# Kernel optimization log

Measured on AMD Instinct MI355X. Metric: run time of the kernel, lower is better.

Reference implementation:

```python
import jax, jax.numpy as jnp
import numpy as np

BIAS = (1, 1)


def setup_inputs() -> dict:
    key = jax.random.key(0)
    k1, k2 = jax.random.split(key)
    B, N = 32, 1024
    c = jax.random.normal(k1, (B, 2 * N), dtype=jnp.float32)
    y = jax.random.randint(k2, (B, N), 0, 2, dtype=jnp.int32)
    return {"c": c, "y": y}


def reference(c, y):
    # split_tensor: even columns -> c1 (scores c_{2r}), odd columns -> s1 (thresholds s_{2r+1})
    c1 = c[:, ::2]   # [B, N]
    s1 = c[:, 1::2]  # [B, N]
    yf = y.astype(jnp.float32)
    y_bar = 1.0 - yf

    y_norm = jnp.sum(yf, axis=1) ** BIAS[0]
    y_bar_norm = jnp.sum(y_bar, axis=1) ** BIAS[1]
    denom = 2.0 * y_norm * y_bar_norm + y_norm * y_norm + y_bar_norm * y_bar_norm

    # pairwise_sub_exp(a, b, x) = sum_{k,l} a_k b_l exp(x_l - x_k)
    #                           = (sum_k a_k e^{-x_k}) * (sum_l b_l e^{x_l})  -- fused, no [B,N,N] materialization
    y_exp_neg_c1 = jnp.sum(yf * jnp.exp(-c1), axis=1)      # sum_k y_k e^{-c1_k}
    ybar_exp_c1 = jnp.sum(y_bar * jnp.exp(c1), axis=1)     # sum_l ybar_l e^{c1_l}
    ybar_exp_neg_s1 = jnp.sum(y_bar * jnp.exp(-s1), axis=1)
    y_exp_s1 = jnp.sum(yf * jnp.exp(s1), axis=1)

    p1 = y_exp_neg_c1 * ybar_exp_c1        # pairwise_sub_exp(y, y_bar, c1)
    p2 = ybar_exp_neg_s1 * y_exp_s1        # pairwise_sub_exp(y_bar, y, s1)
    # valueThreshod_sub_exp(a, x, s) = sum_{r,t} a_r a_t exp(s_t - x_r)
    v1 = y_exp_neg_c1 * y_exp_s1           # valueThreshod_sub_exp(y, c1, s1)
    v2 = ybar_exp_neg_s1 * ybar_exp_c1     # valueThreshod_sub_exp(y_bar, s1, c1)

    return jnp.mean((p1 + p2 + v1 + v2) / denom)
```

## Files before the change

kernel.cpp:

```cpp
#include <hip/hip_runtime.h>

#define NCOLS 1024
#define NROWS 32

__global__ __launch_bounds__(1024) void bpmll_fused_kernel(
    const float* __restrict__ c, const int* __restrict__ y,
    float* __restrict__ out) {
    const int tid = threadIdx.x;
    const int wave = tid >> 6;
    const int lane = tid & 63;
    __shared__ float rowv[NROWS];

    #pragma unroll
    for (int rr = 0; rr < 2; ++rr) {
        const int row = wave * 2 + rr;
        const float4* __restrict__ crow4 =
            reinterpret_cast<const float4*>(c + (size_t)row * 2 * NCOLS);
        const int2* __restrict__ yrow2 =
            reinterpret_cast<const int2*>(y + (size_t)row * NCOLS);

        float sy = 0.f, sA = 0.f, sB = 0.f, sC = 0.f, sD = 0.f;
        #pragma unroll
        for (int k = 0; k < 8; ++k) {
            const int idx = k * 64 + lane;
            const float4 F = crow4[idx];
            const int2  Y = yrow2[idx];
            {
                const bool yy = (Y.x != 0);
                const float e1 = __expf(yy ? -F.x : F.x);
                const float e2 = __expf(yy ?  F.y : -F.y);
                sy += yy ? 1.f : 0.f;
                sA += yy ? e1 : 0.f;
                sD += yy ? e2 : 0.f;
                sC += yy ? 0.f : e1;
                sB += yy ? 0.f : e2;
            }
            {
                const bool yy = (Y.y != 0);
                const float e1 = __expf(yy ? -F.z : F.z);
                const float e2 = __expf(yy ?  F.w : -F.w);
                sy += yy ? 1.f : 0.f;
                sA += yy ? e1 : 0.f;
                sD += yy ? e2 : 0.f;
                sC += yy ? 0.f : e1;
                sB += yy ? 0.f : e2;
            }
        }
        #pragma unroll
        for (int off = 32; off > 0; off >>= 1) {
            sy += __shfl_xor(sy, off);
            sA += __shfl_xor(sA, off);
            sB += __shfl_xor(sB, off);
            sC += __shfl_xor(sC, off);
            sD += __shfl_xor(sD, off);
        }
        if (lane == 0) {
            const float yn  = sy;
            const float ybn = (float)NCOLS - sy;
            const float denom = 2.f * yn * ybn + yn * yn + ybn * ybn;
            rowv[row] = (sA + sB) * (sC + sD) / denom;
        }
    }
    __syncthreads();
    if (tid < 64) {
        float v = (lane < NROWS) ? rowv[lane] : 0.f;
        #pragma unroll
        for (int off = 32; off > 0; off >>= 1) v += __shfl_xor(v, off);
        if (lane == 0) out[0] = v * (1.f / NROWS);
    }
}

extern "C" void kernel_launch(void* const* d_in, const int* in_sizes, int n_in,
                              void* d_out, int out_size, void* d_ws, size_t ws_size,
                              hipStream_t stream) {
    const float* c = (const float*)d_in[0];
    const int*   y = (const int*)d_in[1];
    float* out = (float*)d_out;
    (void)d_ws; (void)ws_size;
    bpmll_fused_kernel<<<1, 1024, 0, stream>>>(c, y, out);
}
```

Baseline: 11.60 us.

## Spread rows across 32 blocks with cooperative grid sync for final mean

Replaces the single 1024-thread block with 32 blocks of 256 threads, one per row, so the loads and exponentials run across many compute units instead of one. Per-row partial sums are reduced through shared memory and written to workspace, then a cooperative grid sync lets block 0 compute the mean. This adds the overhead of a cooperative launch and a grid-wide barrier, which can be costly next to such a small amount of work.

```diff
diff --git a/kernel.cpp b/kernel.cpp
--- a/kernel.cpp
+++ b/kernel.cpp
@@ -1,72 +1,85 @@
 #include <hip/hip_runtime.h>
+#include <hip/hip_cooperative_groups.h>
+
+namespace cg = cooperative_groups;
 
 #define NCOLS 1024
 #define NROWS 32
 
-__global__ __launch_bounds__(1024) void bpmll_fused_kernel(
+__global__ __launch_bounds__(256) void bpmll_coop_kernel(
     const float* __restrict__ c, const int* __restrict__ y,
-    float* __restrict__ out) {
+    float* __restrict__ ws, float* __restrict__ out) {
+    const int row = blockIdx.x;
     const int tid = threadIdx.x;
     const int wave = tid >> 6;
     const int lane = tid & 63;
-    __shared__ float rowv[NROWS];
 
+    const float4* __restrict__ crow4 =
+        reinterpret_cast<const float4*>(c + (size_t)row * 2 * NCOLS);
+    const int2* __restrict__ yrow2 =
+        reinterpret_cast<const int2*>(y + (size_t)row * NCOLS);
+
+    float sy = 0.f, sA = 0.f, sB = 0.f, sC = 0.f, sD = 0.f;
     #pragma unroll
-    for (int rr = 0; rr < 2; ++rr) {
-        const int row = wave * 2 + rr;
-        const float4* __restrict__ crow4 =
-            reinterpret_cast<const float4*>(c + (size_t)row * 2 * NCOLS);
-        const int2* __restrict__ yrow2 =
-            reinterpret_cast<const int2*>(y + (size_t)row * NCOLS);
-
-        float sy = 0.f, sA = 0.f, sB = 0.f, sC = 0.f, sD = 0.f;
-        #pragma unroll
-        for (int k = 0; k < 8; ++k) {
-            const int idx = k * 64 + lane;
-            const float4 F = crow4[idx];
-            const int2  Y = yrow2[idx];
-            {
-                const bool yy = (Y.x != 0);
-                const float e1 = __expf(yy ? -F.x : F.x);
-                const float e2 = __expf(yy ?  F.y : -F.y);
-                sy += yy ? 1.f : 0.f;
-                sA += yy ? e1 : 0.f;
-                sD += yy ? e2 : 0.f;
-                sC += yy ? 0.f : e1;
-                sB += yy ? 0.f : e2;
-            }
-            {
-                const bool yy = (Y.y != 0);
-                const float e1 = __expf(yy ? -F.z : F.z);
-                const float e2 = __expf(yy ?  F.w : -F.w);
-                sy += yy ? 1.f : 0.f;
-                sA += yy ? e1 : 0.f;
-                sD += yy ? e2 : 0.f;
-                sC += yy ? 0.f : e1;
-                sB += yy ? 0.f : e2;
-            }
+    for (int k = 0; k < 2; ++k) {
+        const int idx = k * 256 + tid;
+        const float4 F = crow4[idx];
+        const int2  Y = yrow2[idx];
+        {
+            const bool yy = (Y.x != 0);
+            const float e1 = __expf(yy ? -F.x : F.x);
+            const float e2 = __expf(yy ?  F.y : -F.y);
+            sy += yy ? 1.f : 0.f;
+            sA += yy ? e1 : 0.f;
+            sD += yy ? e2 : 0.f;
+            sC += yy ? 0.f : e1;
+            sB += yy ? 0.f : e2;
         }
-        #pragma unroll
-        for (int off = 32; off > 0; off >>= 1) {
-            sy += __shfl_xor(sy, off);
-            sA += __shfl_xor(sA, off);
-            sB += __shfl_xor(sB, off);
-            sC += __shfl_xor(sC, off);
-            sD += __shfl_xor(sD, off);
-        }
-        if (lane == 0) {
-            const float yn  = sy;
-            const float ybn = (float)NCOLS - sy;
-            const float denom = 2.f * yn * ybn + yn * yn + ybn * ybn;
-            rowv[row] = (sA + sB) * (sC + sD) / denom;
+        {
+            const bool yy = (Y.y != 0);
+            const float e1 = __expf(yy ? -F.z : F.z);
+            const float e2 = __expf(yy ?  F.w : -F.w);
+            sy += yy ? 1.f : 0.f;
+            sA += yy ? e1 : 0.f;
+            sD += yy ? e2 : 0.f;
+            sC += yy ? 0.f : e1;
+            sB += yy ? 0.f : e2;
         }
     }
+    #pragma unroll
+    for (int off = 32; off > 0; off >>= 1) {
+        sy += __shfl_xor(sy, off);
+        sA += __shfl_xor(sA, off);
+        sB += __shfl_xor(sB, off);
+        sC += __shfl_xor(sC, off);
+        sD += __shfl_xor(sD, off);
+    }
+    __shared__ float red[4][5];
+    if (lane == 0) {
+        red[wave][0] = sy; red[wave][1] = sA; red[wave][2] = sB;
+        red[wave][3] = sC; red[wave][4] = sD;
+    }
     __syncthreads();
-    if (tid < 64) {
-        float v = (lane < NROWS) ? rowv[lane] : 0.f;
+    if (tid == 0) {
+        float ty = 0.f, tA = 0.f, tB = 0.f, tC = 0.f, tD = 0.f;
+        #pragma unroll
+        for (int w = 0; w < 4; ++w) {
+            ty += red[w][0]; tA += red[w][1]; tB += red[w][2];
+            tC += red[w][3]; tD += red[w][4];
+        }
+        const float yn  = ty;
+        const float ybn = (float)NCOLS - ty;
+        const float denom = 2.f * yn * ybn + yn * yn + ybn * ybn;
+        ws[row] = (tA + tB) * (tC + tD) / denom;
+    }
+
+    cg::this_grid().sync();
+
+    if (blockIdx.x == 0 && tid < 64) {
+        float v = (tid < NROWS) ? ws[tid] : 0.f;
         #pragma unroll
         for (int off = 32; off > 0; off >>= 1) v += __shfl_xor(v, off);
-        if (lane == 0) out[0] = v * (1.f / NROWS);
+        if (tid == 0) out[0] = v * (1.f / NROWS);
     }
 }
 
@@ -76,6 +89,8 @@
     const float* c = (const float*)d_in[0];
     const int*   y = (const int*)d_in[1];
     float* out = (float*)d_out;
-    (void)d_ws; (void)ws_size;
-    bpmll_fused_kernel<<<1, 1024, 0, stream>>>(c, y, out);
+    float* ws  = (float*)d_ws;
+    void* args[] = {(void*)&c, (void*)&y, (void*)&ws, (void*)&out};
+    hipLaunchCooperativeKernel((void*)bpmll_coop_kernel,
+                               dim3(NROWS), dim3(256), args, 0, stream);
 }
```

Result: slower. 34.01 us (+193.2%).
